# Kernel tuning notes

Measured on AMD Instinct MI355X. Metric: run time of the kernel, lower is better.

Reference implementation:

```python
import jax, jax.numpy as jnp
import numpy as np

N_NODES = 50000
N_EDGES = 800000
IN_CH = 128
HID = 64
HEADS = 2
OUT_CH = 3
N_GRAPHS = 64
NEG_SLOPE = 0.2


def _gatv2(x, src, dst, Wl, Wr, att, bias, heads, out_ch, concat, n_nodes):
    # GATv2Conv (PyG semantics, eval mode, self-loops already appended)
    xl = (x @ Wl).reshape(n_nodes, heads, out_ch)  # lin_l -> source messages
    xr = (x @ Wr).reshape(n_nodes, heads, out_ch)  # lin_r -> target side
    e = jax.nn.leaky_relu(xl[src] + xr[dst], NEG_SLOPE)          # [E, H, C]
    alpha = jnp.einsum('ehc,hc->eh', e, att)                     # [E, H]
    # segment softmax over incoming edges of each target node
    amax = jax.ops.segment_max(alpha, dst, num_segments=n_nodes)  # [N, H]
    ea = jnp.exp(alpha - amax[dst])
    denom = jax.ops.segment_sum(ea, dst, num_segments=n_nodes)
    alpha = ea / (denom[dst] + 1e-16)
    msg = xl[src] * alpha[..., None]                             # [E, H, C]
    out = jax.ops.segment_sum(msg, dst, num_segments=n_nodes)    # [N, H, C]
    out = out.reshape(n_nodes, heads * out_ch) if concat else out.mean(axis=1)
    return out + bias


def setup_inputs() -> dict:
    key = jax.random.key(0)
    ks = jax.random.split(key, 12)
    x = jax.random.normal(ks[0], (N_NODES, IN_CH), dtype=jnp.float32)
    edge_index = jax.random.randint(ks[1], (2, N_EDGES), 0, N_NODES, dtype=jnp.int64 if jax.config.jax_enable_x64 else jnp.int32)
    batch = jnp.sort(jax.random.randint(ks[2], (N_NODES,), 0, N_GRAPHS))
    s = 0.05
    params = {
        'W1l': jax.random.normal(ks[3], (IN_CH, HEADS * HID), dtype=jnp.float32) * s,
        'W1r': jax.random.normal(ks[4], (IN_CH, HEADS * HID), dtype=jnp.float32) * s,
        'att1': jax.random.normal(ks[5], (HEADS, HID), dtype=jnp.float32) * s,
        'b1': jnp.zeros((HEADS * HID,), dtype=jnp.float32),
        'W2l': jax.random.normal(ks[6], (HEADS * HID, OUT_CH), dtype=jnp.float32) * s,
        'W2r': jax.random.normal(ks[7], (HEADS * HID, OUT_CH), dtype=jnp.float32) * s,
        'att2': jax.random.normal(ks[8], (1, OUT_CH), dtype=jnp.float32) * s,
        'b2': jnp.zeros((OUT_CH,), dtype=jnp.float32),
        'Wr1': jax.random.normal(ks[9], (OUT_CH, 64), dtype=jnp.float32) * s,
        'br1': jnp.zeros((64,), dtype=jnp.float32),
        'Wr2': jax.random.normal(ks[10], (64, 3), dtype=jnp.float32) * s,
        'br2': jnp.zeros((3,), dtype=jnp.float32),
    }
    return {'x': x, 'edge_index': edge_index, 'batch': batch, **params}


def reference(x, edge_index, batch, W1l, W1r, att1, b1, W2l, W2r, att2, b2, Wr1, br1, Wr2, br2):
    n = x.shape[0]
    loops = jnp.arange(n, dtype=edge_index.dtype)
    src = jnp.concatenate([edge_index[0], loops])  # add_self_loops=True
    dst = jnp.concatenate([edge_index[1], loops])
    h = _gatv2(x, src, dst, W1l, W1r, att1, b1, HEADS, HID, True, n)
    h = jax.nn.elu(h)
    h = _gatv2(h, src, dst, W2l, W2r, att2, b2, 1, OUT_CH, False, n)
    # global_mean_pool over graphs
    sums = jax.ops.segment_sum(h, batch, num_segments=N_GRAPHS)
    cnt = jax.ops.segment_sum(jnp.ones((n,), h.dtype), batch, num_segments=N_GRAPHS)
    g = sums / jnp.maximum(cnt, 1.0)[:, None]
    g = jax.nn.relu(g @ Wr1 + br1)
    return g @ Wr2 + br2
```

## Files before the change

kernel.cpp:

```cpp
#include <hip/hip_runtime.h>


#define NGRAPH 64
#define LOG2E 1.4426950408889634f

#define DPP_ROR(C, x) \
  __int_as_float(__builtin_amdgcn_update_dpp(0, __float_as_int(x), (0x120 | C), 0xF, 0xF, false))

__device__ __forceinline__ float rowsum16(float v) {
  v += DPP_ROR(8, v);
  v += DPP_ROR(4, v);
  v += DPP_ROR(2, v);
  v += DPP_ROR(1, v);
  return v;
}

__device__ __forceinline__ unsigned bf16rne(float f) {
  unsigned u = __float_as_uint(f);
  return (u + 0x7FFFu + ((u >> 16) & 1u)) >> 16;
}

typedef __attribute__((ext_vector_type(8))) short bf16x8;
typedef __attribute__((ext_vector_type(4))) float f32x4;

__global__ void k_deg(const int* __restrict__ ei, int E, int Et,
                      int* __restrict__ deg, int* __restrict__ rank) {
  int e = blockIdx.x * blockDim.x + threadIdx.x;
  if (e >= Et) return;
  int d = (e < E) ? ei[E + e] : (e - E);
  rank[e] = atomicAdd(&deg[d], 1);
}

__global__ __launch_bounds__(256) void k_scan_part(const int* __restrict__ deg,
                                                   int* __restrict__ bsum, int n) {
  __shared__ int sd[256];
  int t = threadIdx.x;
  int i = blockIdx.x * 1024 + t * 4;
  int s = 0;
  if (i + 4 <= n) {
    int4 d = *(const int4*)&deg[i];
    s = d.x + d.y + d.z + d.w;
  } else {
    for (int j = i; j < min(i + 4, n); ++j) s += deg[j];
  }
  sd[t] = s;
  __syncthreads();
  for (int off = 128; off; off >>= 1) {
    if (t < off) sd[t] += sd[t + off];
    __syncthreads();
  }
  if (t == 0) bsum[blockIdx.x] = sd[0];
}

__global__ __launch_bounds__(64) void k_scan_top(int* __restrict__ bsum, int nb) {
  __shared__ int s[64];
  int t = threadIdx.x;
  s[t] = (t < nb) ? bsum[t] : 0;
  __syncthreads();
  int acc = 0;
  for (int j = 0; j < t; ++j) acc += s[j];
  if (t < nb) bsum[t] = acc;
}

__global__ __launch_bounds__(256) void k_scan_write(const int* __restrict__ deg,
                                                    const int* __restrict__ bsum,
                                                    int* __restrict__ row_ptr, int n) {
  __shared__ int sd[256];
  int t = threadIdx.x;
  int i = blockIdx.x * 1024 + t * 4;
  int4 d = make_int4(0, 0, 0, 0);
  bool full = (i + 4 <= n);
  if (full) d = *(const int4*)&deg[i];
  else {
    if (i + 0 < n) d.x = deg[i + 0];
    if (i + 1 < n) d.y = deg[i + 1];
    if (i + 2 < n) d.z = deg[i + 2];
    if (i + 3 < n) d.w = deg[i + 3];
  }
  int s = d.x + d.y + d.z + d.w;
  sd[t] = s;
  __syncthreads();
  for (int off = 1; off < 256; off <<= 1) {
    int v = (t >= off) ? sd[t - off] : 0;
    __syncthreads();
    sd[t] += v;
    __syncthreads();
  }
  int ex = sd[t] - s + bsum[blockIdx.x];
  int4 r;
  r.x = ex;
  r.y = ex + d.x;
  r.z = r.y + d.y;
  r.w = r.z + d.z;
  if (full) {
    *(int4*)&row_ptr[i] = r;
    if (i + 4 == n) row_ptr[n] = r.w + d.w;
  } else if (i < n) {
    int run = ex;
    int vals[4] = {d.x, d.y, d.z, d.w};
    for (int j = 0; j < 4 && i + j < n; ++j) {
      row_ptr[i + j] = run;
      run += vals[j];
    }
    if (i <= n && i + 4 > n) row_ptr[n] = run;
  }
}

__global__ void k_fill(const int* __restrict__ ei, int E, int Et,
                       const int* __restrict__ row_ptr,
                       const int* __restrict__ rank,
                       int* __restrict__ csr_src) {
  int e = blockIdx.x * blockDim.x + threadIdx.x;
  if (e >= Et) return;
  int s, d;
  if (e < E) { s = ei[e]; d = ei[E + e]; }
  else       { s = e - E; d = s; }
  csr_src[row_ptr[d] + rank[e]] = s;
}

__global__ __launch_bounds__(256) void k_cvt(const float* __restrict__ x,
                                             const float* __restrict__ W1l,
                                             const float* __restrict__ W1r,
                                             unsigned short* __restrict__ xh,
                                             unsigned short* __restrict__ xlo,
                                             unsigned short* __restrict__ wh,
                                             unsigned short* __restrict__ wlo,
                                             int total_x, int xblk) {
  if ((int)blockIdx.x < xblk) {
    int i = (blockIdx.x * 256 + threadIdx.x) * 8;
    if (i + 8 <= total_x) {
      float4 a = *(const float4*)&x[i];
      float4 b = *(const float4*)&x[i + 4];
      float f[8] = {a.x, a.y, a.z, a.w, b.x, b.y, b.z, b.w};
      unsigned hv[8], lv[8];
#pragma unroll
      for (int j = 0; j < 8; ++j) {
        hv[j] = bf16rne(f[j]);
        float r = f[j] - __uint_as_float(hv[j] << 16);
        lv[j] = bf16rne(r);
      }
      uint4 ph, pl;
      ph.x = hv[0] | (hv[1] << 16); ph.y = hv[2] | (hv[3] << 16);
      ph.z = hv[4] | (hv[5] << 16); ph.w = hv[6] | (hv[7] << 16);
      pl.x = lv[0] | (lv[1] << 16); pl.y = lv[2] | (lv[3] << 16);
      pl.z = lv[4] | (lv[5] << 16); pl.w = lv[6] | (lv[7] << 16);
      *(uint4*)&xh[i] = ph;
      *(uint4*)&xlo[i] = pl;
    } else {
      for (int j = i; j < total_x; ++j) {
        float f = x[j];
        unsigned h = bf16rne(f);
        xh[j] = (unsigned short)h;
        xlo[j] = (unsigned short)bf16rne(f - __uint_as_float(h << 16));
      }
    }
  } else {
    int j = ((int)blockIdx.x - xblk) * 256 + threadIdx.x;
    if (j < 256 * 128) {
      int col = j >> 7, k = j & 127;
      float w = (col < 128) ? W1l[k * 128 + col] : W1r[k * 128 + (col - 128)];
      unsigned h = bf16rne(w);
      wh[j] = (unsigned short)h;
      wlo[j] = (unsigned short)bf16rne(w - __uint_as_float(h << 16));
    }
  }
}

__global__ __launch_bounds__(256) void k_gmfma(const unsigned short* __restrict__ xh,
                                               const unsigned short* __restrict__ xlo,
                                               const unsigned short* __restrict__ wh,
                                               const unsigned short* __restrict__ wlo,
                                               unsigned short* __restrict__ outl,
                                               float* __restrict__ outr, int n) {
  int wid = threadIdx.x >> 6;
  int lane = threadIdx.x & 63;
  int lr = lane & 15;
  int lk = (lane >> 4) * 8;
  int r0 = blockIdx.x * 64;
  int wcol = wid * 64;

  int rows[4];
#pragma unroll
  for (int m = 0; m < 4; ++m) rows[m] = min(r0 + m * 16 + lr, n - 1);

  f32x4 acc[4][4] = {};

#pragma unroll
  for (int kc = 0; kc < 4; ++kc) {
    int ko = kc * 32 + lk;
    bf16x8 ah[4], al[4], bh[4], bl[4];
#pragma unroll
    for (int m = 0; m < 4; ++m) {
      ah[m] = *(const bf16x8*)&xh[(size_t)rows[m] * 128 + ko];
      al[m] = *(const bf16x8*)&xlo[(size_t)rows[m] * 128 + ko];
    }
#pragma unroll
    for (int f = 0; f < 4; ++f) {
      int c = wcol + f * 16 + lr;
      bh[f] = *(const bf16x8*)&wh[c * 128 + ko];
      bl[f] = *(const bf16x8*)&wlo[c * 128 + ko];
    }
#pragma unroll
    for (int m = 0; m < 4; ++m)
#pragma unroll
      for (int f = 0; f < 4; ++f) {
        acc[m][f] = __builtin_amdgcn_mfma_f32_16x16x32_bf16(ah[m], bh[f], acc[m][f], 0, 0, 0);
        acc[m][f] = __builtin_amdgcn_mfma_f32_16x16x32_bf16(ah[m], bl[f], acc[m][f], 0, 0, 0);
        acc[m][f] = __builtin_amdgcn_mfma_f32_16x16x32_bf16(al[m], bh[f], acc[m][f], 0, 0, 0);
      }
  }

  int rbase = (lane >> 4) * 4;
  if (wid < 2) {
#pragma unroll
    for (int m = 0; m < 4; ++m)
#pragma unroll
      for (int f = 0; f < 4; ++f) {
        int col = wcol + f * 16 + lr;
#pragma unroll
        for (int i = 0; i < 4; ++i) {
          int row = r0 + m * 16 + rbase + i;
          if (row < n)
            outl[(size_t)row * 128 + col] = (unsigned short)bf16rne(acc[m][f][i]);
        }
      }
  } else {
#pragma unroll
    for (int m = 0; m < 4; ++m)
#pragma unroll
      for (int f = 0; f < 4; ++f) {
        int col = (wid - 2) * 64 + f * 16 + lr;
#pragma unroll
        for (int i = 0; i < 4; ++i) {
          int row = r0 + m * 16 + rbase + i;
          if (row < n)
            outr[(size_t)row * 128 + col] = acc[m][f][i];
        }
      }
  }
}

__global__ __launch_bounds__(256) void k_fused1(const unsigned short* __restrict__ xl,
                                                const float* __restrict__ xr,
                                                const int* __restrict__ row_ptr,
                                                const int* __restrict__ csr_src,
                                                const float* __restrict__ att1,
                                                const float* __restrict__ b1,
                                                const float* __restrict__ W2l,
                                                const float* __restrict__ W2r,
                                                float* __restrict__ xl2,
                                                float* __restrict__ xr2, int n) {
  int wid  = (blockIdx.x * 256 + threadIdx.x) >> 6;
  int lane = threadIdx.x & 63;
  int sub  = lane & 31;
  int node = min(wid * 2 + (lane >> 5), n - 1);
  int ch = sub * 4;
  const char* xlb = (const char*)xl;
  unsigned chb = (unsigned)sub * 8u;
  float4 xrv = *(const float4*)&xr[(size_t)node * 128 + ch];
  float4 atv = *(const float4*)&att1[ch];
  atv.x *= LOG2E; atv.y *= LOG2E; atv.z *= LOG2E; atv.w *= LOG2E;
  int s0 = row_ptr[node];
  int deg = row_ptr[node + 1] - s0;
  int odeg = __shfl_xor(deg, 32);
  int mindeg = min(deg, odeg);
  int maxdeg = max(deg, odeg);
  const int* sp = csr_src + s0;

  float m = -1e30f, l = 0.f;
  float4 acc = make_float4(0.f, 0.f, 0.f, 0.f);

  float t0, t1, t2, t3;
#define UNPACK(dst, q)                                                  \
    dst.x = __uint_as_float(q.x << 16);                                 \
    dst.y = __uint_as_float(q.x & 0xFFFF0000u);                         \
    dst.z = __uint_as_float(q.y << 16);                                 \
    dst.w = __uint_as_float(q.y & 0xFFFF0000u);
#define LOGIT(p, v)                                                     \
    t0 = v.x + xrv.x; t0 = fmaxf(t0, 0.2f * t0);                        \
    t1 = v.y + xrv.y; t1 = fmaxf(t1, 0.2f * t1);                        \
    t2 = v.z + xrv.z; t2 = fmaxf(t2, 0.2f * t2);                        \
    t3 = v.w + xrv.w; t3 = fmaxf(t3, 0.2f * t3);                        \
    p = fmaf(t3, atv.w, fmaf(t2, atv.z, fmaf(t1, atv.y, t0 * atv.x)));

#define BODY(CLAMPED)                                                   \
  {                                                                     \
    int sA, sB, sC, sD;                                                 \
    if (CLAMPED) {                                                      \
      int dm1 = deg - 1;                                                \
      sA = sp[min(e + 0, dm1)];                                         \
      sB = sp[min(e + 1, dm1)];                                         \
      sC = sp[min(e + 2, dm1)];                                         \
      sD = sp[min(e + 3, dm1)];                                         \
    } else {                                                            \
      sA = sp[e + 0]; sB = sp[e + 1]; sC = sp[e + 2]; sD = sp[e + 3];   \
    }                                                                   \
    uint2 qa = *(const uint2*)(xlb + (((unsigned)sA << 8) + chb));      \
    uint2 qb = *(const uint2*)(xlb + (((unsigned)sB << 8) + chb));      \
    uint2 qc = *(const uint2*)(xlb + (((unsigned)sC << 8) + chb));      \
    uint2 qd = *(const uint2*)(xlb + (((unsigned)sD << 8) + chb));      \
    float4 xa, xb, xc, xd;                                              \
    UNPACK(xa, qa) UNPACK(xb, qb) UNPACK(xc, qc) UNPACK(xd, qd)         \
    float pa, pb, pc, pd;                                               \
    LOGIT(pa, xa) LOGIT(pb, xb) LOGIT(pc, xc) LOGIT(pd, xd)             \
    pa = rowsum16(pa);                                                  \
    pb = rowsum16(pb);                                                  \
    pc = rowsum16(pc);                                                  \
    pd = rowsum16(pd);                                                  \
    if (CLAMPED) {                                                      \
      pa = (e + 0 < deg) ? pa : -1e30f;                                 \
      pb = (e + 1 < deg) ? pb : -1e30f;                                 \
      pc = (e + 2 < deg) ? pc : -1e30f;                                 \
      pd = (e + 3 < deg) ? pd : -1e30f;                                 \
    }                                                                   \
    float mn = fmaxf(m, fmaxf(fmaxf(pa, pb), fmaxf(pc, pd)));           \
    float sc = exp2f(m - mn);                                           \
    float wa = exp2f(pa - mn);                                          \
    float wb = exp2f(pb - mn);                                          \
    float wc = exp2f(pc - mn);                                          \
    float wd = exp2f(pd - mn);                                          \
    acc.x = fmaf(wd, xd.x, fmaf(wc, xc.x, fmaf(wb, xb.x, fmaf(wa, xa.x, acc.x * sc)))); \
    acc.y = fmaf(wd, xd.y, fmaf(wc, xc.y, fmaf(wb, xb.y, fmaf(wa, xa.y, acc.y * sc)))); \
    acc.z = fmaf(wd, xd.z, fmaf(wc, xc.z, fmaf(wb, xb.z, fmaf(wa, xa.z, acc.z * sc)))); \
    acc.w = fmaf(wd, xd.w, fmaf(wc, xc.w, fmaf(wb, xb.w, fmaf(wa, xa.w, acc.w * sc)))); \
    l = fmaf(l, sc, wa + wb + wc + wd);                                 \
    m = mn;                                                             \
  }

  int e = 0;
  for (; e + 4 <= mindeg; e += 4) BODY(false)
  for (; e < maxdeg; e += 4) BODY(true)
#undef BODY
#undef LOGIT
#undef UNPACK

  float inv = 1.f / (l + 1e-16f);
  float4 b1v = *(const float4*)&b1[ch];
  float4 h;
  h.x = acc.x * inv + b1v.x; h.x = h.x > 0.f ? h.x : expm1f(h.x);
  h.y = acc.y * inv + b1v.y; h.y = h.y > 0.f ? h.y : expm1f(h.y);
  h.z = acc.z * inv + b1v.z; h.z = h.z > 0.f ? h.z : expm1f(h.z);
  h.w = acc.w * inv + b1v.w; h.w = h.w > 0.f ? h.w : expm1f(h.w);

  float4 u0 = *(const float4*)&W2l[ch * 3 + 0];
  float4 u1 = *(const float4*)&W2l[ch * 3 + 4];
  float4 u2 = *(const float4*)&W2l[ch * 3 + 8];
  float al0 = fmaf(h.w, u2.y, fmaf(h.z, u1.z, fmaf(h.y, u0.w, h.x * u0.x)));
  float al1 = fmaf(h.w, u2.z, fmaf(h.z, u1.w, fmaf(h.y, u1.x, h.x * u0.y)));
  float al2 = fmaf(h.w, u2.w, fmaf(h.z, u2.x, fmaf(h.y, u1.y, h.x * u0.z)));
  float4 v0 = *(const float4*)&W2r[ch * 3 + 0];
  float4 v1 = *(const float4*)&W2r[ch * 3 + 4];
  float4 v2 = *(const float4*)&W2r[ch * 3 + 8];
  float ar0 = fmaf(h.w, v2.y, fmaf(h.z, v1.z, fmaf(h.y, v0.w, h.x * v0.x)));
  float ar1 = fmaf(h.w, v2.z, fmaf(h.z, v1.w, fmaf(h.y, v1.x, h.x * v0.y)));
  float ar2 = fmaf(h.w, v2.w, fmaf(h.z, v2.x, fmaf(h.y, v1.y, h.x * v0.z)));
#pragma unroll
  for (int off = 1; off < 32; off <<= 1) {
    al0 += __shfl_xor(al0, off); al1 += __shfl_xor(al1, off);
    al2 += __shfl_xor(al2, off); ar0 += __shfl_xor(ar0, off);
    ar1 += __shfl_xor(ar1, off); ar2 += __shfl_xor(ar2, off);
  }
  if (sub == 0 && wid * 2 + (lane >> 5) < n) {
    *(float4*)&xl2[node * 4] = make_float4(al0, al1, al2, 0.f);
    *(float4*)&xr2[node * 4] = make_float4(ar0, ar1, ar2, 0.f);
  }
}

__global__ __launch_bounds__(256) void k_fused2(const float* __restrict__ xl2,
                                                const float* __restrict__ xr2,
                                                const int* __restrict__ row_ptr,
                                                const int* __restrict__ csr_src,
                                                const float* __restrict__ att2,
                                                const float* __restrict__ b2,
                                                const int* __restrict__ batch,
                                                float* __restrict__ gsum,
                                                float* __restrict__ gcnt, int n) {
  __shared__ float ls[NGRAPH * 3];
  __shared__ float lc[NGRAPH];
  int t = threadIdx.x;
  for (int i = t; i < NGRAPH * 3; i += 256) ls[i] = 0.f;
  for (int i = t; i < NGRAPH; i += 256) lc[i] = 0.f;
  __syncthreads();

  int node = (blockIdx.x * 256 + t) >> 4;
  int lane = t & 15;
  if (node < n) {
    float4 xrv = *(const float4*)&xr2[node * 4];
    float c0 = att2[0] * LOG2E, c1 = att2[1] * LOG2E, c2 = att2[2] * LOG2E;
    int s0 = row_ptr[node], s1 = row_ptr[node + 1];
    float m = -1e30f, l = 0.f, a0 = 0.f, a1 = 0.f, a2 = 0.f;
    for (int slot = s0 + lane; slot < s1; slot += 16) {
      int s = csr_src[slot];
      float4 xlv = *(const float4*)&xl2[s * 4];
      float t0 = xlv.x + xrv.x; t0 = fmaxf(t0, 0.2f * t0);
      float t1 = xlv.y + xrv.y; t1 = fmaxf(t1, 0.2f * t1);
      float t2 = xlv.z + xrv.z; t2 = fmaxf(t2, 0.2f * t2);
      float p = fmaf(t2, c2, fmaf(t1, c1, t0 * c0));
      float mn = fmaxf(m, p);
      float sc = exp2f(m - mn);
      float w  = exp2f(p - mn);
      a0 = a0 * sc + w * xlv.x;
      a1 = a1 * sc + w * xlv.y;
      a2 = a2 * sc + w * xlv.z;
      l = l * sc + w;
      m = mn;
    }
#define MERGE(C)                                                        \
    {                                                                   \
      float m2 = DPP_ROR(C, m);                                         \
      float l2 = DPP_ROR(C, l);                                         \
      float b0 = DPP_ROR(C, a0);                                        \
      float b1v = DPP_ROR(C, a1);                                       \
      float b2v = DPP_ROR(C, a2);                                       \
      float mn = fmaxf(m, m2);                                          \
      float sA = exp2f(m - mn);                                         \
      float sB = exp2f(m2 - mn);                                        \
      a0 = a0 * sA + b0 * sB;                                           \
      a1 = a1 * sA + b1v * sB;                                          \
      a2 = a2 * sA + b2v * sB;                                          \
      l = l * sA + l2 * sB;                                             \
      m = mn;                                                           \
    }
    MERGE(8) MERGE(4) MERGE(2) MERGE(1)
#undef MERGE
    if (lane == 0) {
      float inv = 1.f / (l + 1e-16f);
      float o0 = a0 * inv + b2[0];
      float o1 = a1 * inv + b2[1];
      float o2 = a2 * inv + b2[2];
      int b = batch[node];
      atomicAdd(&ls[b * 3 + 0], o0);
      atomicAdd(&ls[b * 3 + 1], o1);
      atomicAdd(&ls[b * 3 + 2], o2);
      atomicAdd(&lc[b], 1.f);
    }
  }
  __syncthreads();
  for (int i = t; i < NGRAPH * 3; i += 256)
    if (ls[i] != 0.f) atomicAdd(&gsum[i], ls[i]);
  for (int i = t; i < NGRAPH; i += 256)
    if (lc[i] != 0.f) atomicAdd(&gcnt[i], lc[i]);
}

__global__ __launch_bounds__(64) void k_mlp(const float* __restrict__ gsum,
                                            const float* __restrict__ gcnt,
                                            const float* __restrict__ Wr1,
                                            const float* __restrict__ br1,
                                            const float* __restrict__ Wr2,
                                            const float* __restrict__ br2,
                                            float* __restrict__ out) {
  int t = threadIdx.x;
  if (t >= NGRAPH) return;
  float cnt = fmaxf(gcnt[t], 1.f);
  float g0 = gsum[t * 3 + 0] / cnt;
  float g1 = gsum[t * 3 + 1] / cnt;
  float g2 = gsum[t * 3 + 2] / cnt;
  float o0 = br2[0], o1 = br2[1], o2 = br2[2];
  for (int j = 0; j < 64; ++j) {
    float hj = g0 * Wr1[j] + g1 * Wr1[64 + j] + g2 * Wr1[128 + j] + br1[j];
    hj = fmaxf(hj, 0.f);
    o0 = fmaf(hj, Wr2[j * 3 + 0], o0);
    o1 = fmaf(hj, Wr2[j * 3 + 1], o1);
    o2 = fmaf(hj, Wr2[j * 3 + 2], o2);
  }
  out[t * 3 + 0] = o0;
  out[t * 3 + 1] = o1;
  out[t * 3 + 2] = o2;
}

extern "C" void kernel_launch(void* const* d_in, const int* in_sizes, int n_in,
                              void* d_out, int out_size, void* d_ws, size_t ws_size,
                              hipStream_t stream) {
  const float* x    = (const float*)d_in[0];
  const int*   ei   = (const int*)d_in[1];
  const int*   batch= (const int*)d_in[2];
  const float* W1l  = (const float*)d_in[3];
  const float* W1r  = (const float*)d_in[4];
  const float* att1 = (const float*)d_in[5];
  const float* b1   = (const float*)d_in[6];
  const float* W2l  = (const float*)d_in[7];
  const float* W2r  = (const float*)d_in[8];
  const float* att2 = (const float*)d_in[9];
  const float* b2   = (const float*)d_in[10];
  const float* Wr1  = (const float*)d_in[11];
  const float* br1  = (const float*)d_in[12];
  const float* Wr2  = (const float*)d_in[13];
  const float* br2  = (const float*)d_in[14];
  float* out = (float*)d_out;

  const int N  = in_sizes[0] / 128;
  const int E  = in_sizes[1] / 2;
  const int Et = E + N;
  const int NB = (N + 1023) / 1024;

  char* p = (char*)d_ws;
  auto alloc = [&](size_t bytes) -> char* {
    char* r = p;
    p += (bytes + 255) & ~(size_t)255;
    return r;
  };
  unsigned short* xl1 = (unsigned short*)alloc((size_t)N * 128 * 2);
  float*    xr1    = (float*)alloc((size_t)N * 128 * 4);
  int*      row_ptr= (int*)alloc((size_t)(N + 1) * 4);
  int*      csr_src= (int*)alloc((size_t)Et * 4);
  int*      rank   = (int*)alloc((size_t)Et * 4);
  int*      bsum   = (int*)alloc(64 * 4);
  char*     z0     = p;
  int*      deg    = (int*)alloc((size_t)N * 4);
  float*    gsum   = (float*)alloc(NGRAPH * 3 * 4);
  float*    gcnt   = (float*)alloc(NGRAPH * 4);
  size_t    zbytes = (size_t)(p - z0);
  float*    xl2    = (float*)alloc((size_t)N * 4 * 4);
  float*    xr2    = (float*)alloc((size_t)N * 4 * 4);
  unsigned short* xh  = (unsigned short*)alloc((size_t)N * 128 * 2);
  unsigned short* xlo = (unsigned short*)alloc((size_t)N * 128 * 2);
  unsigned short* wth = (unsigned short*)alloc((size_t)256 * 128 * 2);
  unsigned short* wtl = (unsigned short*)alloc((size_t)256 * 128 * 2);

  hipMemsetAsync(z0, 0, zbytes, stream);
  hipLaunchKernelGGL(k_deg, dim3((Et + 255) / 256), dim3(256), 0, stream,
                     ei, E, Et, deg, rank);
  hipLaunchKernelGGL(k_scan_part, dim3(NB), dim3(256), 0, stream, deg, bsum, N);
  hipLaunchKernelGGL(k_scan_top, dim3(1), dim3(64), 0, stream, bsum, NB);
  hipLaunchKernelGGL(k_scan_write, dim3(NB), dim3(256), 0, stream,
                     deg, bsum, row_ptr, N);
  hipLaunchKernelGGL(k_fill, dim3((Et + 255) / 256), dim3(256), 0, stream,
                     ei, E, Et, row_ptr, rank, csr_src);
  const int total_x = N * 128;
  const int xblk = (total_x + 2047) / 2048;
  const int wblk = (256 * 128 + 255) / 256;
  hipLaunchKernelGGL(k_cvt, dim3(xblk + wblk), dim3(256), 0, stream,
                     x, W1l, W1r, xh, xlo, wth, wtl, total_x, xblk);
  hipLaunchKernelGGL(k_gmfma, dim3((N + 63) / 64), dim3(256), 0, stream,
                     xh, xlo, wth, wtl, xl1, xr1, N);
  int waves1 = (N + 1) / 2;
  hipLaunchKernelGGL(k_fused1, dim3((waves1 * 64 + 255) / 256), dim3(256), 0, stream,
                     xl1, xr1, row_ptr, csr_src, att1, b1, W2l, W2r, xl2, xr2, N);
  hipLaunchKernelGGL(k_fused2, dim3((N * 16 + 255) / 256), dim3(256), 0, stream,
                     xl2, xr2, row_ptr, csr_src, att2, b2, batch, gsum, gcnt, N);
  hipLaunchKernelGGL(k_mlp, dim3(1), dim3(64), 0, stream,
                     gsum, gcnt, Wr1, br1, Wr2, br2, out);
}
```

Before: 277.5 us.

## Pre-pack bf16 split operands into MFMA fragment order and shrink GEMM row tile

The conversion kernel now writes the hi/lo bf16 copies of x and the weights directly in per-lane MFMA fragment order (16-row blocks × 4 k-chunks × 64 lanes × 8). The GEMM then loads each fragment with one contiguous 16-byte load per lane instead of strided row gathers. The GEMM tile also drops from 64 to 32 rows per block, doubling the grid and halving accumulator registers. The aim is better coalescing and higher occupancy in the first-layer projection, at the cost of a padded workspace and more blocks re-reading the weights.

```diff
diff --git a/kernel.cpp b/kernel.cpp
--- a/kernel.cpp
+++ b/kernel.cpp
@@ -121,87 +121,90 @@
 __global__ __launch_bounds__(256) void k_cvt(const float* __restrict__ x,
                                              const float* __restrict__ W1l,
                                              const float* __restrict__ W1r,
-                                             unsigned short* __restrict__ xh,
-                                             unsigned short* __restrict__ xlo,
-                                             unsigned short* __restrict__ wh,
-                                             unsigned short* __restrict__ wlo,
-                                             int total_x, int xblk) {
-  if ((int)blockIdx.x < xblk) {
-    int i = (blockIdx.x * 256 + threadIdx.x) * 8;
-    if (i + 8 <= total_x) {
-      float4 a = *(const float4*)&x[i];
-      float4 b = *(const float4*)&x[i + 4];
-      float f[8] = {a.x, a.y, a.z, a.w, b.x, b.y, b.z, b.w};
-      unsigned hv[8], lv[8];
-#pragma unroll
-      for (int j = 0; j < 8; ++j) {
-        hv[j] = bf16rne(f[j]);
-        float r = f[j] - __uint_as_float(hv[j] << 16);
-        lv[j] = bf16rne(r);
-      }
-      uint4 ph, pl;
-      ph.x = hv[0] | (hv[1] << 16); ph.y = hv[2] | (hv[3] << 16);
-      ph.z = hv[4] | (hv[5] << 16); ph.w = hv[6] | (hv[7] << 16);
-      pl.x = lv[0] | (lv[1] << 16); pl.y = lv[2] | (lv[3] << 16);
-      pl.z = lv[4] | (lv[5] << 16); pl.w = lv[6] | (lv[7] << 16);
-      *(uint4*)&xh[i] = ph;
-      *(uint4*)&xlo[i] = pl;
+                                             unsigned short* __restrict__ xhp,
+                                             unsigned short* __restrict__ xlp,
+                                             unsigned short* __restrict__ whp,
+                                             unsigned short* __restrict__ wlp,
+                                             int n, int RB) {
+  int t = threadIdx.x;
+  int kc = t >> 6;
+  int l = t & 63;
+  int lr = l & 15;
+  int k0 = kc * 32 + (l >> 4) * 8;
+  int b = blockIdx.x;
+  float f[8];
+  if (b < RB) {
+    int row = b * 16 + lr;
+    if (row < n) {
+      float4 a = *(const float4*)&x[(size_t)row * 128 + k0];
+      float4 c = *(const float4*)&x[(size_t)row * 128 + k0 + 4];
+      f[0] = a.x; f[1] = a.y; f[2] = a.z; f[3] = a.w;
+      f[4] = c.x; f[5] = c.y; f[6] = c.z; f[7] = c.w;
     } else {
-      for (int j = i; j < total_x; ++j) {
-        float f = x[j];
-        unsigned h = bf16rne(f);
-        xh[j] = (unsigned short)h;
-        xlo[j] = (unsigned short)bf16rne(f - __uint_as_float(h << 16));
-      }
+#pragma unroll
+      for (int j = 0; j < 8; ++j) f[j] = 0.f;
     }
   } else {
-    int j = ((int)blockIdx.x - xblk) * 256 + threadIdx.x;
-    if (j < 256 * 128) {
-      int col = j >> 7, k = j & 127;
-      float w = (col < 128) ? W1l[k * 128 + col] : W1r[k * 128 + (col - 128)];
-      unsigned h = bf16rne(w);
-      wh[j] = (unsigned short)h;
-      wlo[j] = (unsigned short)bf16rne(w - __uint_as_float(h << 16));
-    }
-  }
-}
-
-__global__ __launch_bounds__(256) void k_gmfma(const unsigned short* __restrict__ xh,
-                                               const unsigned short* __restrict__ xlo,
-                                               const unsigned short* __restrict__ wh,
-                                               const unsigned short* __restrict__ wlo,
+    int col = (b - RB) * 16 + lr;
+#pragma unroll
+    for (int j = 0; j < 8; ++j)
+      f[j] = (col < 128) ? W1l[(size_t)(k0 + j) * 128 + col]
+                         : W1r[(size_t)(k0 + j) * 128 + (col - 128)];
+  }
+  unsigned hv[8], lv[8];
+#pragma unroll
+  for (int j = 0; j < 8; ++j) {
+    hv[j] = bf16rne(f[j]);
+    float r = f[j] - __uint_as_float(hv[j] << 16);
+    lv[j] = bf16rne(r);
+  }
+  uint4 ph, pl;
+  ph.x = hv[0] | (hv[1] << 16); ph.y = hv[2] | (hv[3] << 16);
+  ph.z = hv[4] | (hv[5] << 16); ph.w = hv[6] | (hv[7] << 16);
+  pl.x = lv[0] | (lv[1] << 16); pl.y = lv[2] | (lv[3] << 16);
+  pl.z = lv[4] | (lv[5] << 16); pl.w = lv[6] | (lv[7] << 16);
+  if (b < RB) {
+    size_t slot = (((size_t)b * 4 + kc) * 64 + l) * 8;
+    *(uint4*)&xhp[slot] = ph;
+    *(uint4*)&xlp[slot] = pl;
+  } else {
+    size_t slot = (((size_t)(b - RB) * 4 + kc) * 64 + l) * 8;
+    *(uint4*)&whp[slot] = ph;
+    *(uint4*)&wlp[slot] = pl;
+  }
+}
+
+__global__ __launch_bounds__(256) void k_gmfma(const unsigned short* __restrict__ xhp,
+                                               const unsigned short* __restrict__ xlp,
+                                               const unsigned short* __restrict__ whp,
+                                               const unsigned short* __restrict__ wlp,
                                                unsigned short* __restrict__ outl,
                                                float* __restrict__ outr, int n) {
-  int wid = threadIdx.x >> 6;
+  int w = threadIdx.x >> 6;
   int lane = threadIdx.x & 63;
   int lr = lane & 15;
-  int lk = (lane >> 4) * 8;
-  int r0 = blockIdx.x * 64;
-  int wcol = wid * 64;
-
-  int rows[4];
-#pragma unroll
-  for (int m = 0; m < 4; ++m) rows[m] = min(r0 + m * 16 + lr, n - 1);
-
-  f32x4 acc[4][4] = {};
+  int r0 = blockIdx.x * 32;
+  int rb0 = blockIdx.x * 2;
+
+  f32x4 acc[2][4] = {};
 
 #pragma unroll
   for (int kc = 0; kc < 4; ++kc) {
-    int ko = kc * 32 + lk;
-    bf16x8 ah[4], al[4], bh[4], bl[4];
-#pragma unroll
-    for (int m = 0; m < 4; ++m) {
-      ah[m] = *(const bf16x8*)&xh[(size_t)rows[m] * 128 + ko];
-      al[m] = *(const bf16x8*)&xlo[(size_t)rows[m] * 128 + ko];
+    bf16x8 ah[2], al[2], bh[4], bl[4];
+#pragma unroll
+    for (int m = 0; m < 2; ++m) {
+      size_t slot = (((size_t)(rb0 + m) * 4 + kc) * 64 + lane) * 8;
+      ah[m] = *(const bf16x8*)&xhp[slot];
+      al[m] = *(const bf16x8*)&xlp[slot];
     }
 #pragma unroll
     for (int f = 0; f < 4; ++f) {
-      int c = wcol + f * 16 + lr;
-      bh[f] = *(const bf16x8*)&wh[c * 128 + ko];
-      bl[f] = *(const bf16x8*)&wlo[c * 128 + ko];
-    }
-#pragma unroll
-    for (int m = 0; m < 4; ++m)
+      size_t slot = (((size_t)(w * 4 + f) * 4 + kc) * 64 + lane) * 8;
+      bh[f] = *(const bf16x8*)&whp[slot];
+      bl[f] = *(const bf16x8*)&wlp[slot];
+    }
+#pragma unroll
+    for (int m = 0; m < 2; ++m)
 #pragma unroll
       for (int f = 0; f < 4; ++f) {
         acc[m][f] = __builtin_amdgcn_mfma_f32_16x16x32_bf16(ah[m], bh[f], acc[m][f], 0, 0, 0);
@@ -211,12 +214,12 @@
   }
 
   int rbase = (lane >> 4) * 4;
-  if (wid < 2) {
-#pragma unroll
-    for (int m = 0; m < 4; ++m)
+  if (w < 2) {
+#pragma unroll
+    for (int m = 0; m < 2; ++m)
 #pragma unroll
       for (int f = 0; f < 4; ++f) {
-        int col = wcol + f * 16 + lr;
+        int col = w * 64 + f * 16 + lr;
 #pragma unroll
         for (int i = 0; i < 4; ++i) {
           int row = r0 + m * 16 + rbase + i;
@@ -226,10 +229,10 @@
       }
   } else {
 #pragma unroll
-    for (int m = 0; m < 4; ++m)
+    for (int m = 0; m < 2; ++m)
 #pragma unroll
       for (int f = 0; f < 4; ++f) {
-        int col = (wid - 2) * 64 + f * 16 + lr;
+        int col = (w - 2) * 64 + f * 16 + lr;
 #pragma unroll
         for (int i = 0; i < 4; ++i) {
           int row = r0 + m * 16 + rbase + i;
@@ -492,6 +495,8 @@
   const int E  = in_sizes[1] / 2;
   const int Et = E + N;
   const int NB = (N + 1023) / 1024;
+  const int NB32 = (N + 31) / 32;
+  const int RB = NB32 * 2;
 
   char* p = (char*)d_ws;
   auto alloc = [&](size_t bytes) -> char* {
@@ -512,10 +517,10 @@
   size_t    zbytes = (size_t)(p - z0);
   float*    xl2    = (float*)alloc((size_t)N * 4 * 4);
   float*    xr2    = (float*)alloc((size_t)N * 4 * 4);
-  unsigned short* xh  = (unsigned short*)alloc((size_t)N * 128 * 2);
-  unsigned short* xlo = (unsigned short*)alloc((size_t)N * 128 * 2);
-  unsigned short* wth = (unsigned short*)alloc((size_t)256 * 128 * 2);
-  unsigned short* wtl = (unsigned short*)alloc((size_t)256 * 128 * 2);
+  unsigned short* xhp = (unsigned short*)alloc((size_t)RB * 2048 * 2);
+  unsigned short* xlp = (unsigned short*)alloc((size_t)RB * 2048 * 2);
+  unsigned short* whp = (unsigned short*)alloc((size_t)16 * 2048 * 2);
+  unsigned short* wlp = (unsigned short*)alloc((size_t)16 * 2048 * 2);
 
   hipMemsetAsync(z0, 0, zbytes, stream);
   hipLaunchKernelGGL(k_deg, dim3((Et + 255) / 256), dim3(256), 0, stream,
@@ -526,13 +531,10 @@
                      deg, bsum, row_ptr, N);
   hipLaunchKernelGGL(k_fill, dim3((Et + 255) / 256), dim3(256), 0, stream,
                      ei, E, Et, row_ptr, rank, csr_src);
-  const int total_x = N * 128;
-  const int xblk = (total_x + 2047) / 2048;
-  const int wblk = (256 * 128 + 255) / 256;
-  hipLaunchKernelGGL(k_cvt, dim3(xblk + wblk), dim3(256), 0, stream,
-                     x, W1l, W1r, xh, xlo, wth, wtl, total_x, xblk);
-  hipLaunchKernelGGL(k_gmfma, dim3((N + 63) / 64), dim3(256), 0, stream,
-                     xh, xlo, wth, wtl, xl1, xr1, N);
+  hipLaunchKernelGGL(k_cvt, dim3(RB + 16), dim3(256), 0, stream,
+                     x, W1l, W1r, xhp, xlp, whp, wlp, N, RB);
+  hipLaunchKernelGGL(k_gmfma, dim3(NB32), dim3(256), 0, stream,
+                     xhp, xlp, whp, wlp, xl1, xr1, N);
   int waves1 = (N + 1) / 2;
   hipLaunchKernelGGL(k_fused1, dim3((waves1 * 64 + 255) / 256), dim3(256), 0, stream,
                      xl1, xr1, row_ptr, csr_src, att1, b1, W2l, W2r, xl2, xr2, N);
```

Result: faster. 258.8 us (-6.7%).
